# Performance work log

Measured on AMD Instinct MI355X. Metric: run time of the kernel, lower is better.

The kernel has to match this reference:

```python
import jax, jax.numpy as jnp
import numpy as np
from jax import lax

D = 1024          # d_model
ORDER = 2         # hyena order
FILT = 64         # filter_order (implicit MLP width)
EMB = 3           # positional embedding dim (default)
INNER = D * (ORDER + 1)
DF = D * (ORDER - 1)   # filter d_model
L_MAX = 2048


def setup_inputs() -> dict:
    key = jax.random.key(0)
    ks = jax.random.split(key, 16)
    s = 0.02
    return {
        "u": jax.random.normal(ks[0], (4, L_MAX, D), jnp.float32),
        "in_w": jax.random.normal(ks[1], (D, INNER), jnp.float32) * s,
        "in_b": jnp.zeros((INNER,), jnp.float32),
        "short_w": jax.random.normal(ks[2], (INNER, 3), jnp.float32) * 0.3,
        "short_b": jnp.zeros((INNER,), jnp.float32),
        "mlp_w1": jax.random.normal(ks[3], (EMB, FILT), jnp.float32) * 0.3,
        "mlp_b1": jnp.zeros((FILT,), jnp.float32),
        "mlp_w2": jax.random.normal(ks[4], (FILT, FILT), jnp.float32) * 0.1,
        "mlp_b2": jnp.zeros((FILT,), jnp.float32),
        "mlp_w3": jax.random.normal(ks[5], (FILT, FILT), jnp.float32) * 0.1,
        "mlp_b3": jnp.zeros((FILT,), jnp.float32),
        "mlp_wo": jax.random.normal(ks[6], (FILT, DF), jnp.float32) * 0.1,
        "freq": jnp.ones((1, FILT), jnp.float32),       # shared Sin freq (w=1)
        "filt_bias": jax.random.normal(ks[7], (DF,), jnp.float32),
        "out_w": jax.random.normal(ks[8], (D, D), jnp.float32) * s,
        "out_b": jnp.zeros((D,), jnp.float32),
    }


def _pos_emb(L):
    # PositionalEmbedding(emb_dim=3): t, real/imag of exp(-i f w), bands=(3-1)//2=1
    t = jnp.linspace(0.0, 1.0, L)[:, None]                      # (L,1)
    tr = jnp.linspace(0.0, L - 1.0, L)[:, None]
    w = 2.0 * np.pi * tr / L                                    # (L,1)
    f = jnp.array([1e-4], jnp.float32)[None, :]                  # bands=1
    z = jnp.concatenate([t, jnp.cos(f * w), -jnp.sin(f * w)], axis=-1)  # (L,3)
    return z, t


def _decay(t):
    # ExponentialModulation: target=1e-2, fast=0.3, slow=1.5, shift=0
    max_d = np.log(1e-2) / 0.3
    min_d = np.log(1e-2) / 1.5
    deltas = jnp.linspace(min_d, max_d, DF)[None, :]             # (1,DF)
    return jnp.exp(-t * jnp.abs(deltas))                         # (L,DF)


def reference(u, in_w, in_b, short_w, short_b, mlp_w1, mlp_b1, mlp_w2, mlp_b2,
              mlp_w3, mlp_b3, mlp_wo, freq, filt_bias, out_w, out_b):
    B, L, _ = u.shape
    # in_proj: b l d -> b l (3d) -> b (3d) l
    up = jnp.einsum('bld,de->ble', u, in_w) + in_b
    up = up.transpose(0, 2, 1)                                   # (B, INNER, L)
    # depthwise short conv, kernel 3, padding 2 both sides, then [:L]
    uc = lax.conv_general_dilated(up, short_w[:, None, :], (1,), [(2, 2)],
                                  feature_group_count=INNER,
                                  dimension_numbers=('NCH', 'OIH', 'NCH'))
    uc = uc[..., :L] + short_b[None, :, None]
    x0, x1, v = uc[:, :D], uc[:, D:2 * D], uc[:, 2 * D:]
    # implicit long filter k(L): pos-emb -> Sin MLP (shared freq) -> modulation
    z, t = _pos_emb(L)
    h = jnp.sin(freq * (z @ mlp_w1 + mlp_b1))
    h = jnp.sin(freq * (h @ mlp_w2 + mlp_b2))
    h = jnp.sin(freq * (h @ mlp_w3 + mlp_b3))
    h = h @ mlp_wo                                               # (L, DF)
    k = (h * _decay(t)).T                                        # (DF, L) == (D, L) for order=2
    # hyena recurrence: order-1 = 1 gated fft-conv step
    vx = v * x1                                                  # (B, D, L)
    n = 2 * L
    y = jnp.fft.irfft(jnp.fft.rfft(vx, n=n) * jnp.fft.rfft(k, n=n), n=n)[..., :L]
    v = y + vx * filt_bias[None, :, None]
    # final gate + out_proj
    yv = (v * x0).transpose(0, 2, 1)                             # (B, L, D)
    return jnp.einsum('bld,de->ble', yv, out_w) + out_b
```

## Files before the change

### kernel.cpp

```cpp
#include <hip/hip_runtime.h>
#include <math.h>

#define M_PIf 3.14159265358979323846f
#define MIND (-3.0701134573253936f)
#define MAXD (-15.350567286626968f)

typedef __attribute__((ext_vector_type(8))) _Float16 f16x8;
typedef __attribute__((ext_vector_type(4))) float f32x4;
typedef __attribute__((ext_vector_type(8))) unsigned short u16x8;

#define GLDS(g, l) __builtin_amdgcn_global_load_lds(                         \
    (const __attribute__((address_space(1))) void*)(g),                      \
    (__attribute__((address_space(3))) void*)(l), 16, 0, 0)

__device__ __forceinline__ unsigned short f2h(float x) {
    return __builtin_bit_cast(unsigned short, (_Float16)x);
}
__device__ __forceinline__ float h2f(unsigned short h) {
    return (float)__builtin_bit_cast(_Float16, h);
}

__global__ __launch_bounds__(256) void split_kernel(
    const float* __restrict__ in, unsigned short* __restrict__ out, int n4)
{
    int i = blockIdx.x * 256 + threadIdx.x;
    if (i >= n4) return;
    float4 v = ((const float4*)in)[i];
    ushort4 h;
    h.x = f2h(v.x); h.y = f2h(v.y); h.z = f2h(v.z); h.w = f2h(v.w);
    ((ushort4*)out)[i] = h;
}

__global__ __launch_bounds__(256) void tsplit_kernel(
    const float* __restrict__ in, unsigned short* __restrict__ out,
    int R, int C)
{
    __shared__ float t[32][33];
    const int r0 = blockIdx.y * 32, c0 = blockIdx.x * 32;
    const int tx = threadIdx.x & 31, ty = threadIdx.x >> 5;
#pragma unroll
    for (int q = 0; q < 4; ++q) {
        int r = ty + q * 8;
        t[r][tx] = in[(size_t)(r0 + r) * C + c0 + tx];
    }
    __syncthreads();
#pragma unroll
    for (int q = 0; q < 4; ++q) {
        int cc = ty + q * 8;
        out[(size_t)(c0 + cc) * R + r0 + tx] = f2h(t[tx][cc]);
    }
}

__global__ __launch_bounds__(256) void t16_kernel(
    const unsigned short* __restrict__ in, unsigned short* __restrict__ out)
{
    __shared__ unsigned short t[64][66];
    const int b = blockIdx.z;
    const int d0 = blockIdx.y * 64, l0 = blockIdx.x * 64;
    const int tid = threadIdx.x;
    const int rr = tid >> 4, cc = (tid & 15) * 4;
#pragma unroll
    for (int p = 0; p < 4; ++p) {
        int r = p * 16 + rr;
        ushort4 v = *(const ushort4*)&in[((size_t)b * 1024 + d0 + r) * 2048 + l0 + cc];
        t[cc + 0][r] = v.x; t[cc + 1][r] = v.y; t[cc + 2][r] = v.z; t[cc + 3][r] = v.w;
    }
    __syncthreads();
#pragma unroll
    for (int p = 0; p < 4; ++p) {
        int r = p * 16 + rr;
        ushort4 o;
        o.x = t[r][cc + 0]; o.y = t[r][cc + 1]; o.z = t[r][cc + 2]; o.w = t[r][cc + 3];
        *(ushort4*)&out[((size_t)b * 2048 + l0 + r) * 1024 + d0 + cc] = o;
    }
}

template <int TRANS_OUT>
__global__ __launch_bounds__(256, 4) void gemm_f16_kernel(
    const unsigned short* __restrict__ A, const unsigned short* __restrict__ B,
    const float* __restrict__ bias, void* __restrict__ outp)
{
    __shared__ char smem[32768];
    const int tid = threadIdx.x;
    const int wave = tid >> 6, lane = tid & 63;
    const int n0 = blockIdx.x * 128, m0 = blockIdx.y * 128;
    const int wm = wave >> 1, wn = wave & 1;

    f32x4 acc[4][4] = {};

    const int srow = lane >> 2;
    const int scol_sw = (((lane & 3) ^ ((lane >> 3) & 3))) * 16;

    auto stage = [&](int buf, int t) {
        const int k0 = t * 32;
        char* base = smem + buf * 16384;
#pragma unroll
        for (int ld = 0; ld < 2; ++ld) {
            const int rchunk = wave * 32 + ld * 16;
            const int r = rchunk + srow;
            GLDS((const char*)(A + (size_t)(m0 + r) * 1024 + k0) + scol_sw,
                 base + 0 * 8192 + rchunk * 64);
            GLDS((const char*)(B + (size_t)(n0 + r) * 1024 + k0) + scol_sw,
                 base + 1 * 8192 + rchunk * 64);
        }
    };

    stage(0, 0);
    asm volatile("s_waitcnt vmcnt(0)");
    __syncthreads();
    int cur = 0;
    const int rr = lane & 15;
    const int gg_sw = (((lane >> 4) ^ ((rr >> 1) & 3))) * 16;
    for (int t = 0; t < 32; ++t) {
        if (t < 31) stage(cur ^ 1, t + 1);
        const char* b = smem + cur * 16384;
        f16x8 ah[4], bh[4];
#pragma unroll
        for (int i = 0; i < 4; ++i) {
            ah[i] = *(const f16x8*)(b + 0 * 8192 + (wm * 64 + i * 16 + rr) * 64 + gg_sw);
            bh[i] = *(const f16x8*)(b + 1 * 8192 + (wn * 64 + i * 16 + rr) * 64 + gg_sw);
        }
#pragma unroll
        for (int i = 0; i < 4; ++i)
#pragma unroll
            for (int j = 0; j < 4; ++j)
                acc[i][j] = __builtin_amdgcn_mfma_f32_16x16x32_f16(ah[i], bh[j], acc[i][j], 0, 0, 0);
        __syncthreads();
        cur ^= 1;
    }

    const int c = lane & 15, g4 = lane >> 4;
    if (TRANS_OUT) {
        unsigned short* up = (unsigned short*)outp;
        const int bidx = m0 >> 11;
        const int lbase = (m0 & 2047) + wm * 64 + g4 * 4;
#pragma unroll
        for (int j = 0; j < 4; ++j) {
            const int e = n0 + wn * 64 + j * 16 + c;
            const float bv = bias[e];
            unsigned short* dst = up + ((size_t)bidx * 3072 + e) * 2048 + lbase;
#pragma unroll
            for (int i = 0; i < 4; ++i) {
                ushort4 o;
                o.x = f2h(acc[i][j][0] + bv);
                o.y = f2h(acc[i][j][1] + bv);
                o.z = f2h(acc[i][j][2] + bv);
                o.w = f2h(acc[i][j][3] + bv);
                *(ushort4*)(dst + i * 16) = o;
            }
        }
    } else {
        float* op = (float*)outp;
#pragma unroll
        for (int j = 0; j < 4; ++j) {
            const int col = n0 + wn * 64 + j * 16 + c;
            const float bv = bias[col];
#pragma unroll
            for (int i = 0; i < 4; ++i) {
                const int row = m0 + wm * 64 + i * 16 + g4 * 4;
#pragma unroll
                for (int r = 0; r < 4; ++r)
                    op[(size_t)(row + r) * 1024 + col] = acc[i][j][r] + bv;
            }
        }
    }
}

__global__ __launch_bounds__(256) void filt_kernel(
    const float* __restrict__ w1, const float* __restrict__ b1,
    const float* __restrict__ w2, const float* __restrict__ b2,
    const float* __restrict__ w3, const float* __restrict__ b3,
    const float* __restrict__ wo, const float* __restrict__ freq,
    float* __restrict__ kbuf)
{
    __shared__ float ha[8][65], hb[8][65];
    const int l0 = blockIdx.x * 8;
    const int tid = threadIdx.x;
    const int uu = tid & 63, lq = tid >> 6;
#pragma unroll
    for (int p = 0; p < 2; ++p) {
        int ll = lq + p * 4;
        int l = l0 + ll;
        float t = (float)l * (1.0f / 2047.0f);
        float ang = 1e-4f * (2.0f * M_PIf) * ((float)l / 2048.0f);
        float pre = t * w1[uu] + cosf(ang) * w1[64 + uu] - sinf(ang) * w1[128 + uu] + b1[uu];
        ha[ll][uu] = sinf(freq[uu] * pre);
    }
    __syncthreads();
#pragma unroll
    for (int p = 0; p < 2; ++p) {
        int ll = lq + p * 4;
        float s = b2[uu];
#pragma unroll
        for (int i = 0; i < 64; ++i) s += ha[ll][i] * w2[i * 64 + uu];
        hb[ll][uu] = sinf(freq[uu] * s);
    }
    __syncthreads();
#pragma unroll
    for (int p = 0; p < 2; ++p) {
        int ll = lq + p * 4;
        float s = b3[uu];
#pragma unroll
        for (int i = 0; i < 64; ++i) s += hb[ll][i] * w3[i * 64 + uu];
        ha[ll][uu] = sinf(freq[uu] * s);
    }
    __syncthreads();

    float acc[4][8] = {};
    for (int i = 0; i < 64; ++i) {
        float wv[4];
#pragma unroll
        for (int q = 0; q < 4; ++q) wv[q] = wo[i * 1024 + tid + 256 * q];
#pragma unroll
        for (int l = 0; l < 8; ++l) {
            float hv = ha[l][i];
#pragma unroll
            for (int q = 0; q < 4; ++q) acc[q][l] += hv * wv[q];
        }
    }
    const float span = (MAXD - MIND) * (1.0f / 1023.0f);
#pragma unroll
    for (int q = 0; q < 4; ++q) {
        int dd = tid + 256 * q;
        float ad = fabsf(MIND + span * (float)dd);
#pragma unroll
        for (int l = 0; l < 8; ++l) {
            float t = (float)(l0 + l) * (1.0f / 2047.0f);
            kbuf[(size_t)dd * 2048 + l0 + l] = acc[q][l] * expf(-t * ad);
        }
    }
}

__device__ __forceinline__ void conv3_chunk(
    const unsigned short* __restrict__ row, int l0,
    float wa, float wb, float wc, float sbv, float out[8])
{
    f16x8 m = *(const f16x8*)(row + l0);
    float e[10];
    if (l0 > 0) {
        ushort2 p = *(const ushort2*)(row + l0 - 2);
        e[0] = h2f(p.x); e[1] = h2f(p.y);
    } else {
        e[0] = 0.f; e[1] = 0.f;
    }
#pragma unroll
    for (int i = 0; i < 8; ++i) e[2 + i] = (float)m[i];
#pragma unroll
    for (int i = 0; i < 8; ++i)
        out[i] = wa * e[i] + wb * e[i + 1] + wc * e[i + 2] + sbv;
}

__global__ __launch_bounds__(256, 2) void conv_kernel(
    const unsigned short* __restrict__ up_t, const float* __restrict__ kbuf,
    const float* __restrict__ sw, const float* __restrict__ sb,
    const float* __restrict__ fbias, unsigned short* __restrict__ yv)
{
    __shared__ char smem[27712];
#define VH(bb) ((unsigned short*)(smem + (bb) * 4608))
#define X0(bb) ((unsigned short*)(smem + 17472 + (bb) * 5120))
    int* wpk = (int*)(smem + 9216);

    const int d = blockIdx.x;
    const int bqa = blockIdx.y * 2;
    const int tid = threadIdx.x;

    const float* kr = kbuf + (size_t)d * 2048;
    for (int xc = tid * 4; xc < 2064; xc += 1024) {
        int4 w4 = {0, 0, 0, 0};
        if (xc <= 2044) {
            const float4 fv = *(const float4*)&kr[2044 - xc];
            const float e = (xc <= 2040) ? kr[2043 - xc] : 0.f;
            w4.x = (int)((unsigned)f2h(fv.w) | ((unsigned)f2h(fv.z) << 16));
            w4.y = (int)((unsigned)f2h(fv.z) | ((unsigned)f2h(fv.y) << 16));
            w4.z = (int)((unsigned)f2h(fv.y) | ((unsigned)f2h(fv.x) << 16));
            w4.w = (int)((unsigned)f2h(fv.x) | ((unsigned)f2h(e)    << 16));
        }
        *(int4*)&wpk[xc] = w4;
    }

    const float w1a = sw[(1024 + d) * 3 + 0], w1b = sw[(1024 + d) * 3 + 1], w1c = sw[(1024 + d) * 3 + 2];
    const float w2a = sw[(2048 + d) * 3 + 0], w2b = sw[(2048 + d) * 3 + 1], w2c = sw[(2048 + d) * 3 + 2];
    const float w0a = sw[d * 3 + 0], w0b = sw[d * 3 + 1], w0c = sw[d * 3 + 2];
    const float sb1 = sb[1024 + d], sb2 = sb[2048 + d], sb0 = sb[d];
    const int l0 = tid * 8;
#pragma unroll
    for (int bb = 0; bb < 2; ++bb) {
        const int b = bqa + bb;
        const unsigned short* rx1 = up_t + ((size_t)(b * 3072) + 1024 + d) * 2048;
        const unsigned short* rv  = up_t + ((size_t)(b * 3072) + 2048 + d) * 2048;
        const unsigned short* r0  = up_t + ((size_t)(b * 3072) + d) * 2048;
        float x1v[8], vv[8], x0v[8];
        conv3_chunk(rx1, l0, w1a, w1b, w1c, sb1, x1v);
        conv3_chunk(rv,  l0, w2a, w2b, w2c, sb2, vv);
        conv3_chunk(r0,  l0, w0a, w0b, w0c, sb0, x0v);
        u16x8 o;
#pragma unroll
        for (int i = 0; i < 8; ++i) o[i] = f2h(vv[i] * x1v[i]);
        *(u16x8*)(VH(bb) + 240 + l0) = o;
        const int xo = l0 + 4 * (l0 >> 4);
        ushort4 p1, p2;
        p1.x = f2h(x0v[0]); p1.y = f2h(x0v[1]); p1.z = f2h(x0v[2]); p1.w = f2h(x0v[3]);
        p2.x = f2h(x0v[4]); p2.y = f2h(x0v[5]); p2.z = f2h(x0v[6]); p2.w = f2h(x0v[7]);
        *(ushort4*)(X0(bb) + xo) = p1;
        *(ushort4*)(X0(bb) + xo + 4) = p2;
        if (tid < 30) {
            u16x8 z = {};
            *(u16x8*)(VH(bb) + tid * 8) = z;
        }
    }
    __syncthreads();

    const int wv = tid >> 6, lane = tid & 63;
    const int row = lane & 15;
    const int sseg = lane >> 4;
    f32x4 acc[2][2] = {};
#pragma unroll
    for (int gi = 0; gi < 2; ++gi) {
        const int g = gi ? (7 - wv) : wv;
        const int tmax = 8 * g + 8;
        int xA = 2031 - row + 8 * sseg;
        int xB = 224 + 256 * g + 16 * row + 8 * sseg;
        for (int t = 0; t < tmax; ++t) {
            int4 avh;
            avh.x = wpk[xA];     avh.y = wpk[xA + 2];
            avh.z = wpk[xA + 4]; avh.w = wpk[xA + 6];
            f16x8 ah = __builtin_bit_cast(f16x8, avh);
#pragma unroll
            for (int bb = 0; bb < 2; ++bb) {
                f16x8 bh = *(const f16x8*)(VH(bb) + xB);
                acc[gi][bb] = __builtin_amdgcn_mfma_f32_16x16x32_f16(ah, bh, acc[gi][bb], 0, 0, 0);
            }
            xA -= 32;
            xB -= 32;
        }
    }

    const float fb = fbias[d];
#pragma unroll
    for (int gi = 0; gi < 2; ++gi) {
        const int g = gi ? (7 - wv) : wv;
        const int lb = 256 * g + 16 * row + 4 * sseg;
#pragma unroll
        for (int bb = 0; bb < 2; ++bb) {
            ushort4 vhq = *(const ushort4*)(VH(bb) + 240 + lb);
            ushort4 x0q = *(const ushort4*)(X0(bb) + lb + 4 * (lb >> 4));
            f32x4 a = acc[gi][bb];
            ushort4 o;
            o.x = f2h((a[0] + h2f(vhq.x) * fb) * h2f(x0q.x));
            o.y = f2h((a[1] + h2f(vhq.y) * fb) * h2f(x0q.y));
            o.z = f2h((a[2] + h2f(vhq.z) * fb) * h2f(x0q.z));
            o.w = f2h((a[3] + h2f(vhq.w) * fb) * h2f(x0q.w));
            *(ushort4*)&yv[((size_t)((bqa + bb) * 1024) + d) * 2048 + lb] = o;
        }
    }
#undef VH
#undef X0
}

extern "C" void kernel_launch(void* const* d_in, const int* in_sizes, int n_in,
                              void* d_out, int out_size, void* d_ws, size_t ws_size,
                              hipStream_t stream) {
    (void)in_sizes; (void)n_in; (void)out_size; (void)ws_size;
    const float* u         = (const float*)d_in[0];
    const float* in_w      = (const float*)d_in[1];
    const float* in_b      = (const float*)d_in[2];
    const float* short_w   = (const float*)d_in[3];
    const float* short_b   = (const float*)d_in[4];
    const float* mlp_w1    = (const float*)d_in[5];
    const float* mlp_b1    = (const float*)d_in[6];
    const float* mlp_w2    = (const float*)d_in[7];
    const float* mlp_b2    = (const float*)d_in[8];
    const float* mlp_w3    = (const float*)d_in[9];
    const float* mlp_b3    = (const float*)d_in[10];
    const float* mlp_wo    = (const float*)d_in[11];
    const float* freq      = (const float*)d_in[12];
    const float* filt_bias = (const float*)d_in[13];
    const float* out_w     = (const float*)d_in[14];
    const float* out_b     = (const float*)d_in[15];
    float* out = (float*)d_out;

    char* ws = (char*)d_ws;
    const size_t MB = 1024 * 1024;
    unsigned short* up_t = (unsigned short*)ws;
    unsigned short* yvh  = (unsigned short*)(ws + 48 * MB);
    unsigned short* yvt  = (unsigned short*)(ws + 64 * MB);
    unsigned short* w2t  = (unsigned short*)(ws + 80 * MB);
    float*          kbuf = (float*)(ws + 82 * MB);
    unsigned short* uh   = (unsigned short*)(ws + 90 * MB);
    unsigned short* w1t  = (unsigned short*)(ws + 106 * MB);

    hipLaunchKernelGGL(split_kernel, dim3(8192), dim3(256), 0, stream,
                       u, uh, 8192 * 1024 / 4);
    hipLaunchKernelGGL(tsplit_kernel, dim3(96, 32), dim3(256), 0, stream,
                       in_w, w1t, 1024, 3072);
    hipLaunchKernelGGL(filt_kernel, dim3(256), dim3(256), 0, stream,
                       mlp_w1, mlp_b1, mlp_w2, mlp_b2, mlp_w3, mlp_b3, mlp_wo, freq, kbuf);
    hipLaunchKernelGGL((gemm_f16_kernel<1>), dim3(24, 64), dim3(256), 0, stream,
                       uh, w1t, in_b, (void*)up_t);
    hipLaunchKernelGGL(conv_kernel, dim3(1024, 2), dim3(256), 0, stream,
                       up_t, kbuf, short_w, short_b, filt_bias, yvh);
    hipLaunchKernelGGL(t16_kernel, dim3(32, 16, 4), dim3(256), 0, stream,
                       yvh, yvt);
    hipLaunchKernelGGL(tsplit_kernel, dim3(32, 32), dim3(256), 0, stream,
                       out_w, w2t, 1024, 1024);
    hipLaunchKernelGGL((gemm_f16_kernel<0>), dim3(8, 64), dim3(256), 0, stream,
                       yvt, w2t, out_b, (void*)out);
}
```

Measured before the change: 176.6 us.

## Merge prep and transpose kernels into fused launches, raise conv occupancy, unroll MFMA loop

Three independent preprocessing kernels (u fp16 cast, in_w transpose-cast, filter MLP) are merged into one prep_kernel that dispatches on block index. The yv transpose and out_w transpose-cast are likewise merged into one post_kernel. This cuts the launch count from eight to five and lets small jobs share the GPU with one another. Separately, conv_kernel's launch bounds go from 2 to 4 waves per SIMD and its MFMA inner loop is unrolled by two, which may limit registers or cause spills.

```diff
diff --git a/kernel.cpp b/kernel.cpp
--- a/kernel.cpp
+++ b/kernel.cpp
@@ -20,58 +20,146 @@
     return (float)__builtin_bit_cast(_Float16, h);
 }
 
-__global__ __launch_bounds__(256) void split_kernel(
-    const float* __restrict__ in, unsigned short* __restrict__ out, int n4)
+__global__ __launch_bounds__(256) void prep_kernel(
+    const float* __restrict__ u, unsigned short* __restrict__ uh,
+    const float* __restrict__ in_w, unsigned short* __restrict__ w1t,
+    const float* __restrict__ w1, const float* __restrict__ b1,
+    const float* __restrict__ w2, const float* __restrict__ b2,
+    const float* __restrict__ w3, const float* __restrict__ b3,
+    const float* __restrict__ wo, const float* __restrict__ freq,
+    float* __restrict__ kbuf)
 {
-    int i = blockIdx.x * 256 + threadIdx.x;
-    if (i >= n4) return;
-    float4 v = ((const float4*)in)[i];
-    ushort4 h;
-    h.x = f2h(v.x); h.y = f2h(v.y); h.z = f2h(v.z); h.w = f2h(v.w);
-    ((ushort4*)out)[i] = h;
-}
-
-__global__ __launch_bounds__(256) void tsplit_kernel(
-    const float* __restrict__ in, unsigned short* __restrict__ out,
-    int R, int C)
+    __shared__ char sm[4352];
+    const int bid = blockIdx.x;
+    const int tid = threadIdx.x;
+
+    if (bid < 8192) {
+        const int i = bid * 256 + tid;
+        float4 v = ((const float4*)u)[i];
+        ushort4 h;
+        h.x = f2h(v.x); h.y = f2h(v.y); h.z = f2h(v.z); h.w = f2h(v.w);
+        ((ushort4*)uh)[i] = h;
+    } else if (bid < 11264) {
+        float (*t)[33] = (float(*)[33])sm;
+        const int idx = bid - 8192;
+        const int bx = idx % 96, by = idx / 96;
+        const int r0 = by * 32, c0 = bx * 32;
+        const int tx = tid & 31, ty = tid >> 5;
+#pragma unroll
+        for (int q = 0; q < 4; ++q) {
+            int r = ty + q * 8;
+            t[r][tx] = in_w[(size_t)(r0 + r) * 3072 + c0 + tx];
+        }
+        __syncthreads();
+#pragma unroll
+        for (int q = 0; q < 4; ++q) {
+            int cc = ty + q * 8;
+            w1t[(size_t)(c0 + cc) * 1024 + r0 + tx] = f2h(t[tx][cc]);
+        }
+    } else {
+        float (*ha)[65] = (float(*)[65])sm;
+        float (*hb)[65] = (float(*)[65])(sm + 2080);
+        const int l0 = (bid - 11264) * 8;
+        const int uu = tid & 63, lq = tid >> 6;
+#pragma unroll
+        for (int p = 0; p < 2; ++p) {
+            int ll = lq + p * 4;
+            int l = l0 + ll;
+            float t = (float)l * (1.0f / 2047.0f);
+            float ang = 1e-4f * (2.0f * M_PIf) * ((float)l / 2048.0f);
+            float pre = t * w1[uu] + cosf(ang) * w1[64 + uu] - sinf(ang) * w1[128 + uu] + b1[uu];
+            ha[ll][uu] = sinf(freq[uu] * pre);
+        }
+        __syncthreads();
+#pragma unroll
+        for (int p = 0; p < 2; ++p) {
+            int ll = lq + p * 4;
+            float s = b2[uu];
+#pragma unroll
+            for (int i = 0; i < 64; ++i) s += ha[ll][i] * w2[i * 64 + uu];
+            hb[ll][uu] = sinf(freq[uu] * s);
+        }
+        __syncthreads();
+#pragma unroll
+        for (int p = 0; p < 2; ++p) {
+            int ll = lq + p * 4;
+            float s = b3[uu];
+#pragma unroll
+            for (int i = 0; i < 64; ++i) s += hb[ll][i] * w3[i * 64 + uu];
+            ha[ll][uu] = sinf(freq[uu] * s);
+        }
+        __syncthreads();
+
+        float acc[4][8] = {};
+        for (int i = 0; i < 64; ++i) {
+            float wv[4];
+#pragma unroll
+            for (int q = 0; q < 4; ++q) wv[q] = wo[i * 1024 + tid + 256 * q];
+#pragma unroll
+            for (int l = 0; l < 8; ++l) {
+                float hv = ha[l][i];
+#pragma unroll
+                for (int q = 0; q < 4; ++q) acc[q][l] += hv * wv[q];
+            }
+        }
+        const float span = (MAXD - MIND) * (1.0f / 1023.0f);
+#pragma unroll
+        for (int q = 0; q < 4; ++q) {
+            int dd = tid + 256 * q;
+            float ad = fabsf(MIND + span * (float)dd);
+#pragma unroll
+            for (int l = 0; l < 8; ++l) {
+                float t = (float)(l0 + l) * (1.0f / 2047.0f);
+                kbuf[(size_t)dd * 2048 + l0 + l] = acc[q][l] * expf(-t * ad);
+            }
+        }
+    }
+}
+
+__global__ __launch_bounds__(256) void post_kernel(
+    const unsigned short* __restrict__ yvh, unsigned short* __restrict__ yvt,
+    const float* __restrict__ out_w, unsigned short* __restrict__ w2t)
 {
-    __shared__ float t[32][33];
-    const int r0 = blockIdx.y * 32, c0 = blockIdx.x * 32;
-    const int tx = threadIdx.x & 31, ty = threadIdx.x >> 5;
-#pragma unroll
-    for (int q = 0; q < 4; ++q) {
-        int r = ty + q * 8;
-        t[r][tx] = in[(size_t)(r0 + r) * C + c0 + tx];
-    }
-    __syncthreads();
-#pragma unroll
-    for (int q = 0; q < 4; ++q) {
-        int cc = ty + q * 8;
-        out[(size_t)(c0 + cc) * R + r0 + tx] = f2h(t[tx][cc]);
-    }
-}
-
-__global__ __launch_bounds__(256) void t16_kernel(
-    const unsigned short* __restrict__ in, unsigned short* __restrict__ out)
-{
-    __shared__ unsigned short t[64][66];
-    const int b = blockIdx.z;
-    const int d0 = blockIdx.y * 64, l0 = blockIdx.x * 64;
+    __shared__ char sm[8448];
+    const int bid = blockIdx.x;
     const int tid = threadIdx.x;
-    const int rr = tid >> 4, cc = (tid & 15) * 4;
-#pragma unroll
-    for (int p = 0; p < 4; ++p) {
-        int r = p * 16 + rr;
-        ushort4 v = *(const ushort4*)&in[((size_t)b * 1024 + d0 + r) * 2048 + l0 + cc];
-        t[cc + 0][r] = v.x; t[cc + 1][r] = v.y; t[cc + 2][r] = v.z; t[cc + 3][r] = v.w;
-    }
-    __syncthreads();
-#pragma unroll
-    for (int p = 0; p < 4; ++p) {
-        int r = p * 16 + rr;
-        ushort4 o;
-        o.x = t[r][cc + 0]; o.y = t[r][cc + 1]; o.z = t[r][cc + 2]; o.w = t[r][cc + 3];
-        *(ushort4*)&out[((size_t)b * 2048 + l0 + r) * 1024 + d0 + cc] = o;
+    if (bid < 2048) {
+        unsigned short (*t)[66] = (unsigned short(*)[66])sm;
+        const int l0 = (bid & 31) * 64;
+        const int d0 = ((bid >> 5) & 15) * 64;
+        const int b  = bid >> 9;
+        const int rr = tid >> 4, cc = (tid & 15) * 4;
+#pragma unroll
+        for (int p = 0; p < 4; ++p) {
+            int r = p * 16 + rr;
+            ushort4 v = *(const ushort4*)&yvh[((size_t)b * 1024 + d0 + r) * 2048 + l0 + cc];
+            t[cc + 0][r] = v.x; t[cc + 1][r] = v.y; t[cc + 2][r] = v.z; t[cc + 3][r] = v.w;
+        }
+        __syncthreads();
+#pragma unroll
+        for (int p = 0; p < 4; ++p) {
+            int r = p * 16 + rr;
+            ushort4 o;
+            o.x = t[r][cc + 0]; o.y = t[r][cc + 1]; o.z = t[r][cc + 2]; o.w = t[r][cc + 3];
+            *(ushort4*)&yvt[((size_t)b * 2048 + l0 + r) * 1024 + d0 + cc] = o;
+        }
+    } else {
+        float (*t)[33] = (float(*)[33])sm;
+        const int idx = bid - 2048;
+        const int bx = idx & 31, by = idx >> 5;
+        const int r0 = by * 32, c0 = bx * 32;
+        const int tx = tid & 31, ty = tid >> 5;
+#pragma unroll
+        for (int q = 0; q < 4; ++q) {
+            int r = ty + q * 8;
+            t[r][tx] = out_w[(size_t)(r0 + r) * 1024 + c0 + tx];
+        }
+        __syncthreads();
+#pragma unroll
+        for (int q = 0; q < 4; ++q) {
+            int cc = ty + q * 8;
+            w2t[(size_t)(c0 + cc) * 1024 + r0 + tx] = f2h(t[tx][cc]);
+        }
     }
 }
 
@@ -162,71 +250,6 @@
                 for (int r = 0; r < 4; ++r)
                     op[(size_t)(row + r) * 1024 + col] = acc[i][j][r] + bv;
             }
-        }
-    }
-}
-
-__global__ __launch_bounds__(256) void filt_kernel(
-    const float* __restrict__ w1, const float* __restrict__ b1,
-    const float* __restrict__ w2, const float* __restrict__ b2,
-    const float* __restrict__ w3, const float* __restrict__ b3,
-    const float* __restrict__ wo, const float* __restrict__ freq,
-    float* __restrict__ kbuf)
-{
-    __shared__ float ha[8][65], hb[8][65];
-    const int l0 = blockIdx.x * 8;
-    const int tid = threadIdx.x;
-    const int uu = tid & 63, lq = tid >> 6;
-#pragma unroll
-    for (int p = 0; p < 2; ++p) {
-        int ll = lq + p * 4;
-        int l = l0 + ll;
-        float t = (float)l * (1.0f / 2047.0f);
-        float ang = 1e-4f * (2.0f * M_PIf) * ((float)l / 2048.0f);
-        float pre = t * w1[uu] + cosf(ang) * w1[64 + uu] - sinf(ang) * w1[128 + uu] + b1[uu];
-        ha[ll][uu] = sinf(freq[uu] * pre);
-    }
-    __syncthreads();
-#pragma unroll
-    for (int p = 0; p < 2; ++p) {
-        int ll = lq + p * 4;
-        float s = b2[uu];
-#pragma unroll
-        for (int i = 0; i < 64; ++i) s += ha[ll][i] * w2[i * 64 + uu];
-        hb[ll][uu] = sinf(freq[uu] * s);
-    }
-    __syncthreads();
-#pragma unroll
-    for (int p = 0; p < 2; ++p) {
-        int ll = lq + p * 4;
-        float s = b3[uu];
-#pragma unroll
-        for (int i = 0; i < 64; ++i) s += hb[ll][i] * w3[i * 64 + uu];
-        ha[ll][uu] = sinf(freq[uu] * s);
-    }
-    __syncthreads();
-
-    float acc[4][8] = {};
-    for (int i = 0; i < 64; ++i) {
-        float wv[4];
-#pragma unroll
-        for (int q = 0; q < 4; ++q) wv[q] = wo[i * 1024 + tid + 256 * q];
-#pragma unroll
-        for (int l = 0; l < 8; ++l) {
-            float hv = ha[l][i];
-#pragma unroll
-            for (int q = 0; q < 4; ++q) acc[q][l] += hv * wv[q];
-        }
-    }
-    const float span = (MAXD - MIND) * (1.0f / 1023.0f);
-#pragma unroll
-    for (int q = 0; q < 4; ++q) {
-        int dd = tid + 256 * q;
-        float ad = fabsf(MIND + span * (float)dd);
-#pragma unroll
-        for (int l = 0; l < 8; ++l) {
-            float t = (float)(l0 + l) * (1.0f / 2047.0f);
-            kbuf[(size_t)dd * 2048 + l0 + l] = acc[q][l] * expf(-t * ad);
         }
     }
 }
@@ -250,7 +273,7 @@
         out[i] = wa * e[i] + wb * e[i + 1] + wc * e[i + 2] + sbv;
 }
 
-__global__ __launch_bounds__(256, 2) void conv_kernel(
+__global__ __launch_bounds__(256, 4) void conv_kernel(
     const unsigned short* __restrict__ up_t, const float* __restrict__ kbuf,
     const float* __restrict__ sw, const float* __restrict__ sb,
     const float* __restrict__ fbias, unsigned short* __restrict__ yv)
@@ -320,7 +343,7 @@
         const int tmax = 8 * g + 8;
         int xA = 2031 - row + 8 * sseg;
         int xB = 224 + 256 * g + 16 * row + 8 * sseg;
-        for (int t = 0; t < tmax; ++t) {
+        auto step = [&]() {
             int4 avh;
             avh.x = wpk[xA];     avh.y = wpk[xA + 2];
             avh.z = wpk[xA + 4]; avh.w = wpk[xA + 6];
@@ -332,7 +355,8 @@
             }
             xA -= 32;
             xB -= 32;
-        }
+        };
+        for (int t = 0; t < tmax; t += 2) { step(); step(); }
     }
 
     const float fb = fbias[d];
@@ -389,20 +413,15 @@
     unsigned short* uh   = (unsigned short*)(ws + 90 * MB);
     unsigned short* w1t  = (unsigned short*)(ws + 106 * MB);
 
-    hipLaunchKernelGGL(split_kernel, dim3(8192), dim3(256), 0, stream,
-                       u, uh, 8192 * 1024 / 4);
-    hipLaunchKernelGGL(tsplit_kernel, dim3(96, 32), dim3(256), 0, stream,
-                       in_w, w1t, 1024, 3072);
-    hipLaunchKernelGGL(filt_kernel, dim3(256), dim3(256), 0, stream,
+    hipLaunchKernelGGL(prep_kernel, dim3(11520), dim3(256), 0, stream,
+                       u, uh, in_w, w1t,
                        mlp_w1, mlp_b1, mlp_w2, mlp_b2, mlp_w3, mlp_b3, mlp_wo, freq, kbuf);
     hipLaunchKernelGGL((gemm_f16_kernel<1>), dim3(24, 64), dim3(256), 0, stream,
                        uh, w1t, in_b, (void*)up_t);
     hipLaunchKernelGGL(conv_kernel, dim3(1024, 2), dim3(256), 0, stream,
                        up_t, kbuf, short_w, short_b, filt_bias, yvh);
-    hipLaunchKernelGGL(t16_kernel, dim3(32, 16, 4), dim3(256), 0, stream,
-                       yvh, yvt);
-    hipLaunchKernelGGL(tsplit_kernel, dim3(32, 32), dim3(256), 0, stream,
-                       out_w, w2t, 1024, 1024);
+    hipLaunchKernelGGL(post_kernel, dim3(3072), dim3(256), 0, stream,
+                       yvh, yvt, out_w, w2t);
     hipLaunchKernelGGL((gemm_f16_kernel<0>), dim3(8, 64), dim3(256), 0, stream,
                        yvt, w2t, out_b, (void*)out);
 }
```

After: 176.1 us. Within noise of the previous version (-0.2%).
